# Kernel tuning notes

Hardware: AMD Instinct MI355X
Metric: run time of the kernel (lower is better)

The kernel has to match this reference:

```python
import jax, jax.numpy as jnp
import numpy as np

# CSV_Architecture_v2 layout (per frame, 130 floats):
#   hand 0 block: [0]=handedness label, [1]=handedness prob, [2:65]=21*3 coords
#   hand 1 block: [65]=handedness label, [66]=handedness prob, [67:130]=coords
POS0, PROB0 = 0, 1
POS1, PROB1 = 65, 66
HAND_LEN = 65
FRAME_LEN = 2 * HAND_LEN


def _build_swap_pattern():
    all_idxs = np.arange(FRAME_LEN)
    idxs_0 = np.arange(0, HAND_LEN)
    idxs_1 = np.arange(HAND_LEN, FRAME_LEN)
    all_idxs[idxs_0], all_idxs[idxs_1] = all_idxs[idxs_1].copy(), all_idxs[idxs_0].copy()
    return jnp.asarray(all_idxs, dtype=jnp.int32)


def setup_inputs() -> dict:
    key = jax.random.key(0)
    B, S = 256, 1024
    X = jax.random.normal(key, (B, S, FRAME_LEN), dtype=jnp.float32)
    return {"X": X, "swap_pattern": _build_swap_pattern()}


def reference(X, swap_pattern):
    # Per-frame handedness labels / probabilities.
    h0 = X[..., POS0]
    h1 = X[..., POS1]
    p0 = X[..., PROB0]
    p1 = X[..., PROB1]

    nan0 = jnp.isnan(h0)
    nan1 = jnp.isnan(h1)
    no_nan = jnp.logical_and(~nan0, ~nan1)

    one = jnp.float32(1.0)
    zero = jnp.float32(0.0)

    # skip1: hands already ordered (right label > left label)
    skip1 = h1 > h0
    # skip2: both predictions NaN -> no hands detected
    skip2 = jnp.logical_and(nan0, nan1)
    # skip3: only hand 1 present, labeled right (==1)
    skip3 = jnp.logical_and(nan0, h1 == one)
    # skip4: only hand 0 present, labeled left (==0)
    skip4 = jnp.logical_and(nan1, h0 == zero)
    eq = h0 == h1
    # skip5: both labeled left, position-0 hand has higher prob
    skip5 = no_nan & eq & (h0 == zero) & (p0 > p1)
    # skip6: both labeled right, position-1 hand has higher prob
    skip6 = no_nan & eq & (h0 == one) & (p0 < p1)

    skip = skip1 | skip2 | skip3 | skip4 | skip5 | skip6

    # Vectorized replacement of nested tf.map_fn: gather-permute the frame
    # representation where a swap is required.
    swapped = X[..., swap_pattern]  # [B, S, FRAME_LEN]
    return jnp.where(skip[..., None], X, swapped)
```

## Files before the change

kernel.cpp:

```cpp
#include <hip/hip_runtime.h>

constexpr int FRAME_LEN = 130;
constexpr int HALF      = 65;
constexpr int BLOCK     = 256;
constexpr int FPB       = 32;
constexpr int CHUNK_F   = FPB * FRAME_LEN;
constexpr int CHUNK_V4  = CHUNK_F / 4;

__device__ __forceinline__ int div130(int idx) {
    return (int)(((unsigned)idx * 8067u) >> 20);
}

__global__ __launch_bounds__(BLOCK, 8)
void hand_sorter_kernel(const float* __restrict__ X, float* __restrict__ out,
                        int n_frames) {
    __shared__ float s_buf[CHUNK_F];
    __shared__ unsigned char s_skip[FPB];

    const int t = threadIdx.x;
    const long long frame0 = (long long)blockIdx.x * FPB;
    const long long rem = (long long)n_frames - frame0;
    const int frames_here = rem < (long long)FPB ? (int)rem : FPB;
    const int nf = frames_here * FRAME_LEN;
    const int n4 = (nf + 3) >> 2;
    const long long base = frame0 * (long long)FRAME_LEN;
    const float4* __restrict__ Xv = (const float4*)(X + base);
    float4* __restrict__ Ov = (float4*)(out + base);

    for (int i = t; i < n4; i += BLOCK) {
        *(float4*)(s_buf + 4 * i) = Xv[i];
    }
    __syncthreads();

    if (t < frames_here) {
        const float* fr = s_buf + t * FRAME_LEN;
        const float h0 = fr[0];
        const float p0 = fr[1];
        const float h1 = fr[HALF];
        const float p1 = fr[HALF + 1];
        const bool nan0 = (h0 != h0);
        const bool nan1 = (h1 != h1);
        const bool no_nan = !nan0 && !nan1;
        const bool eq = (h0 == h1);
        const bool skip =
            (h1 > h0) ||
            (nan0 && nan1) ||
            (nan0 && (h1 == 1.0f)) ||
            (nan1 && (h0 == 0.0f)) ||
            (no_nan && eq && (h0 == 0.0f) && (p0 > p1)) ||
            (no_nan && eq && (h0 == 1.0f) && (p0 < p1));
        s_skip[t] = (unsigned char)skip;
    }
    __syncthreads();

    for (int i = t; i < n4; i += BLOCK) {
        const int idx = 4 * i;
        float4 v;
        float* vp = (float*)&v;
        if (idx + 3 < nf) {
#pragma unroll
            for (int e = 0; e < 4; ++e) {
                const int ide = idx + e;
                const int fl = div130(ide);
                const int jj = ide - fl * FRAME_LEN;
                int sj = jj + (s_skip[fl] ? 0 : HALF);
                if (sj >= FRAME_LEN) sj -= FRAME_LEN;
                vp[e] = s_buf[fl * FRAME_LEN + sj];
            }
            Ov[i] = v;
        } else {
            for (int e = 0; e < 4; ++e) {
                const int ide = idx + e;
                if (ide < nf) {
                    const int fl = div130(ide);
                    const int jj = ide - fl * FRAME_LEN;
                    int sj = jj + (s_skip[fl] ? 0 : HALF);
                    if (sj >= FRAME_LEN) sj -= FRAME_LEN;
                    out[base + ide] = s_buf[fl * FRAME_LEN + sj];
                }
            }
        }
    }
}

extern "C" void kernel_launch(void* const* d_in, const int* in_sizes, int n_in,
                              void* d_out, int out_size, void* d_ws, size_t ws_size,
                              hipStream_t stream) {
    const float* X = (const float*)d_in[0];
    float* out = (float*)d_out;
    const int n_frames = in_sizes[0] / FRAME_LEN;
    const int n_blocks = (n_frames + FPB - 1) / FPB;
    hand_sorter_kernel<<<n_blocks, BLOCK, 0, stream>>>(X, out, n_frames);
}
```

Measured before the change: 239.8 us.

## Gather directly from global memory, drop LDS staging, use nontemporal stores

Removes the shared-memory staging of each frame chunk. Each thread now reads its permuted elements straight from global memory, relying on cache for reuse, and writes float4 outputs with nontemporal stores. Frames per block is doubled, and the per-slot frame/offset is stepped incrementally instead of divided each time. The trade-off is scalar, uncoalesced-ish global gathers in place of vector loads plus LDS reads, and the output depends on L1/L2 hits.

Measured after the change: 244.0 us. No clear change (+1.8%).

```diff
diff --git a/kernel.cpp b/kernel.cpp
--- a/kernel.cpp
+++ b/kernel.cpp
@@ -3,37 +3,53 @@
 constexpr int FRAME_LEN = 130;
 constexpr int HALF      = 65;
 constexpr int BLOCK     = 256;
-constexpr int FPB       = 32;
+constexpr int FPB       = 64;
 constexpr int CHUNK_F   = FPB * FRAME_LEN;
-constexpr int CHUNK_V4  = CHUNK_F / 4;
+constexpr int NSLOT     = CHUNK_F / 4;
+constexpr int KFULL     = NSLOT / BLOCK;
+constexpr int NTAIL     = NSLOT - KFULL * BLOCK;
+
+typedef float f4 __attribute__((ext_vector_type(4)));
 
 __device__ __forceinline__ int div130(int idx) {
-    return (int)(((unsigned)idx * 8067u) >> 20);
+    return (int)(((unsigned)idx * 129056u) >> 24);
+}
+
+__device__ __forceinline__ void do_slot(const float* __restrict__ Xb,
+                                        float* __restrict__ Ob,
+                                        const int* __restrict__ s_rot,
+                                        int i, int fl, int r0, int fB) {
+    int j2 = r0 + 2, fB2 = fB, flB = fl;
+    if (j2 >= FRAME_LEN) { j2 -= FRAME_LEN; fB2 += FRAME_LEN; flB = fl + 1; }
+    const int j3 = j2 + 1;
+    const int rotA = s_rot[fl];
+    const int rotB = s_rot[flB];
+    int s0 = r0 + rotA;     if (s0 >= FRAME_LEN) s0 -= FRAME_LEN;
+    int s1 = r0 + 1 + rotA; if (s1 >= FRAME_LEN) s1 -= FRAME_LEN;
+    int s2 = j2 + rotB;     if (s2 >= FRAME_LEN) s2 -= FRAME_LEN;
+    int s3 = j3 + rotB;     if (s3 >= FRAME_LEN) s3 -= FRAME_LEN;
+    f4 v;
+    v.x = Xb[fB + s0];
+    v.y = Xb[fB + s1];
+    v.z = Xb[fB2 + s2];
+    v.w = Xb[fB2 + s3];
+    __builtin_nontemporal_store(v, (f4*)Ob + i);
 }
 
 __global__ __launch_bounds__(BLOCK, 8)
 void hand_sorter_kernel(const float* __restrict__ X, float* __restrict__ out,
                         int n_frames) {
-    __shared__ float s_buf[CHUNK_F];
-    __shared__ unsigned char s_skip[FPB];
-
+    __shared__ int s_rot[FPB + 1];
     const int t = threadIdx.x;
     const long long frame0 = (long long)blockIdx.x * FPB;
     const long long rem = (long long)n_frames - frame0;
     const int frames_here = rem < (long long)FPB ? (int)rem : FPB;
-    const int nf = frames_here * FRAME_LEN;
-    const int n4 = (nf + 3) >> 2;
     const long long base = frame0 * (long long)FRAME_LEN;
-    const float4* __restrict__ Xv = (const float4*)(X + base);
-    float4* __restrict__ Ov = (float4*)(out + base);
-
-    for (int i = t; i < n4; i += BLOCK) {
-        *(float4*)(s_buf + 4 * i) = Xv[i];
-    }
-    __syncthreads();
+    const float* __restrict__ Xb = X + base;
+    float* __restrict__ Ob = out + base;
 
     if (t < frames_here) {
-        const float* fr = s_buf + t * FRAME_LEN;
+        const float* fr = Xb + t * FRAME_LEN;
         const float h0 = fr[0];
         const float p0 = fr[1];
         const float h1 = fr[HALF];
@@ -49,36 +65,35 @@
             (nan1 && (h0 == 0.0f)) ||
             (no_nan && eq && (h0 == 0.0f) && (p0 > p1)) ||
             (no_nan && eq && (h0 == 1.0f) && (p0 < p1));
-        s_skip[t] = (unsigned char)skip;
+        s_rot[t] = skip ? 0 : HALF;
     }
     __syncthreads();
 
-    for (int i = t; i < n4; i += BLOCK) {
-        const int idx = 4 * i;
-        float4 v;
-        float* vp = (float*)&v;
-        if (idx + 3 < nf) {
-#pragma unroll
-            for (int e = 0; e < 4; ++e) {
-                const int ide = idx + e;
-                const int fl = div130(ide);
-                const int jj = ide - fl * FRAME_LEN;
-                int sj = jj + (s_skip[fl] ? 0 : HALF);
-                if (sj >= FRAME_LEN) sj -= FRAME_LEN;
-                vp[e] = s_buf[fl * FRAME_LEN + sj];
-            }
-            Ov[i] = v;
-        } else {
-            for (int e = 0; e < 4; ++e) {
-                const int ide = idx + e;
-                if (ide < nf) {
-                    const int fl = div130(ide);
-                    const int jj = ide - fl * FRAME_LEN;
-                    int sj = jj + (s_skip[fl] ? 0 : HALF);
-                    if (sj >= FRAME_LEN) sj -= FRAME_LEN;
-                    out[base + ide] = s_buf[fl * FRAME_LEN + sj];
-                }
-            }
+    if (frames_here == FPB) {
+        int idx = 4 * t;
+        int fl = div130(idx);
+        int r0 = idx - fl * FRAME_LEN;
+        int fB = fl * FRAME_LEN;
+#pragma unroll 4
+        for (int k = 0; k < KFULL; ++k) {
+            do_slot(Xb, Ob, s_rot, t + k * BLOCK, fl, r0, fB);
+            r0 += 114; fl += 7; fB += 7 * FRAME_LEN;
+            if (r0 >= FRAME_LEN) { r0 -= FRAME_LEN; ++fl; fB += FRAME_LEN; }
+        }
+        if (t < NTAIL) {
+            const int i = KFULL * BLOCK + t;
+            const int id2 = 4 * i;
+            const int f2 = div130(id2);
+            do_slot(Xb, Ob, s_rot, i, f2, id2 - f2 * FRAME_LEN, f2 * FRAME_LEN);
+        }
+    } else {
+        const int nf = frames_here * FRAME_LEN;
+        for (int idx = t; idx < nf; idx += BLOCK) {
+            const int fl = div130(idx);
+            const int jj = idx - fl * FRAME_LEN;
+            int sj = jj + s_rot[fl];
+            if (sj >= FRAME_LEN) sj -= FRAME_LEN;
+            Ob[idx] = Xb[fl * FRAME_LEN + sj];
         }
     }
 }
```
